# Performance work log

Measured on AMD Instinct MI355X. Metric: run time of the kernel, lower is better.

## Reference

```python
import jax, jax.numpy as jnp
import numpy as np

N_NODES = 100000
N_EDGES = 500000
N_GRAPHS = 64
IN_DIM = 512
HID = 256
N_REL = 16


def setup_inputs() -> dict:
    key = jax.random.key(0)
    ks = jax.random.split(key, 14)
    s = 0.02
    inp = {}
    inp["node_feats"] = jax.random.normal(ks[0], (N_NODES, IN_DIM), dtype=jnp.float32)
    inp["edge_index"] = jax.random.randint(ks[1], (2, N_EDGES), 0, N_NODES, dtype=jnp.int64)
    inp["batch_idx"] = jnp.sort(jax.random.randint(ks[2], (N_NODES,), 0, N_GRAPHS, dtype=jnp.int64))
    # GraphConv layer 0: in 512 -> 256; layers 1,2: 256 -> 256
    inp["W_rel0"] = jax.random.normal(ks[3], (IN_DIM, HID), dtype=jnp.float32) * s
    inp["W_root0"] = jax.random.normal(ks[4], (IN_DIM, HID), dtype=jnp.float32) * s
    inp["b0"] = jnp.zeros((HID,), dtype=jnp.float32)
    inp["W_rel1"] = jax.random.normal(ks[5], (HID, HID), dtype=jnp.float32) * s
    inp["W_root1"] = jax.random.normal(ks[6], (HID, HID), dtype=jnp.float32) * s
    inp["b1"] = jnp.zeros((HID,), dtype=jnp.float32)
    inp["W_rel2"] = jax.random.normal(ks[7], (HID, HID), dtype=jnp.float32) * s
    inp["W_root2"] = jax.random.normal(ks[8], (HID, HID), dtype=jnp.float32) * s
    inp["b2"] = jnp.zeros((HID,), dtype=jnp.float32)
    # edge head: concat(src, dst) -> relations
    inp["W_edge"] = jax.random.normal(ks[9], (2 * HID, N_REL), dtype=jnp.float32) * s
    inp["b_edge"] = jnp.zeros((N_REL,), dtype=jnp.float32)
    return inp


def _graph_conv(x, src, dst, W_rel, W_root, b):
    # PyG GraphConv: out_i = W_root x_i + W_rel * sum_{j in N(i)} x_j + b
    agg = jax.ops.segment_sum(x[src], dst, num_segments=x.shape[0])  # [N, d_in]
    return agg @ W_rel + x @ W_root + b


def reference(node_feats, edge_index, batch_idx,
              W_rel0, W_root0, b0, W_rel1, W_root1, b1, W_rel2, W_root2, b2,
              W_edge, b_edge):
    src, dst = edge_index[0], edge_index[1]
    # 3 GraphConv layers with ReLU (dropout is identity at inference)
    x = jax.nn.relu(_graph_conv(node_feats, src, dst, W_rel0, W_root0, b0))
    x = jax.nn.relu(_graph_conv(x, src, dst, W_rel1, W_root1, b1))
    x = jax.nn.relu(_graph_conv(x, src, dst, W_rel2, W_root2, b2))
    # edge head: gather src/dst embeddings, concat, linear
    edge_feats = jnp.concatenate([x[src], x[dst]], axis=1)  # [E, 2*HID]
    edge_logits = edge_feats @ W_edge + b_edge              # [E, N_REL]
    # global mean pool per graph
    sums = jax.ops.segment_sum(x, batch_idx, num_segments=N_GRAPHS)  # [G, HID]
    counts = jax.ops.segment_sum(jnp.ones((x.shape[0], 1), x.dtype), batch_idx, num_segments=N_GRAPHS)
    graph_embed = sums / jnp.maximum(counts, 1.0)
    return edge_logits, graph_embed
```

## Files before the change

kernel.cpp:

```cpp
#include <hip/hip_runtime.h>

#define N_NODES 100000
#define N_EDGES 500000
#define N_GRAPHS 64
#define IN_DIM 512
#define HID 256
#define NREL 16

using short8 = __attribute__((ext_vector_type(8))) short;
using f32x4  = __attribute__((ext_vector_type(4))) float;

__device__ __forceinline__ unsigned short f2bf(float f) {
    union { float f; unsigned u; } v; v.f = f;
    unsigned u = v.u;
    unsigned r = u + 0x7FFF + ((u >> 16) & 1);
    return (unsigned short)(r >> 16);
}
__device__ __forceinline__ float bf2f(unsigned short h) {
    union { unsigned u; float f; } v; v.u = ((unsigned)h) << 16;
    return v.f;
}

__device__ __forceinline__ void gload_lds16(const unsigned short* g, unsigned short* l) {
    __builtin_amdgcn_global_load_lds(
        (const __attribute__((address_space(1))) void*)(g),
        (__attribute__((address_space(3))) void*)(l), 16, 0, 0);
}

__global__ void k_f2bf(const float* __restrict__ in, unsigned short* __restrict__ out, int n8) {
    int i = blockIdx.x * 256 + threadIdx.x;
    if (i >= n8) return;
    const float4* p = (const float4*)in + (size_t)i * 2;
    float4 a = p[0], b = p[1];
    ushort4 u0, u1;
    u0.x = f2bf(a.x); u0.y = f2bf(a.y); u0.z = f2bf(a.z); u0.w = f2bf(a.w);
    u1.x = f2bf(b.x); u1.y = f2bf(b.y); u1.z = f2bf(b.z); u1.w = f2bf(b.w);
    ushort4* q = (ushort4*)out + (size_t)i * 2;
    q[0] = u0; q[1] = u1;
}

__global__ void k_makeWt(const float* __restrict__ Wrel, const float* __restrict__ Wroot,
                         unsigned short* __restrict__ Wt, int K) {
    int n = blockIdx.x;
    const float* Wsrc = (n < HID) ? Wrel : Wroot;
    int col = n & (HID - 1);
    for (int k = threadIdx.x; k < K; k += 256)
        Wt[(size_t)n * K + k] = f2bf(Wsrc[(size_t)k * HID + col]);
}

__global__ void k_makeWe2T(const float* __restrict__ We, unsigned short* __restrict__ We2T) {
    int idx = blockIdx.x * 256 + threadIdx.x;
    if (idx >= 32 * 256) return;
    int r = idx >> 8, k = idx & 255;
    float v = (r < 16) ? We[k * NREL + r] : We[(256 + k) * NREL + (r - 16)];
    We2T[idx] = f2bf(v);
}

__global__ void k_hist(const int* __restrict__ dstArr, int* __restrict__ counts) {
    int i = blockIdx.x * 256 + threadIdx.x;
    if (i < N_EDGES) atomicAdd(&counts[dstArr[i]], 1);
}

__global__ void k_scanA(const int* __restrict__ counts, int* __restrict__ bsum) {
    __shared__ int ws[4];
    int i = blockIdx.x * 256 + threadIdx.x;
    int v = (i < N_NODES) ? counts[i] : 0;
    for (int o = 32; o; o >>= 1) v += __shfl_down(v, o, 64);
    if ((threadIdx.x & 63) == 0) ws[threadIdx.x >> 6] = v;
    __syncthreads();
    if (threadIdx.x == 0) bsum[blockIdx.x] = ws[0] + ws[1] + ws[2] + ws[3];
}

__global__ void k_scanB(int* __restrict__ bsum, int nb) {
    __shared__ int buf[512];
    int t = threadIdx.x;
    for (int i = t; i < nb; i += 256) buf[i] = bsum[i];
    __syncthreads();
    if (t == 0) { int s = 0; for (int i = 0; i < nb; ++i) { int x = buf[i]; buf[i] = s; s += x; } }
    __syncthreads();
    for (int i = t; i < nb; i += 256) bsum[i] = buf[i];
}

__global__ void k_scanC(const int* __restrict__ counts, const int* __restrict__ bsum,
                        int* __restrict__ offsets, int* __restrict__ cur) {
    __shared__ int ws[4];
    int i = blockIdx.x * 256 + threadIdx.x;
    int lane = threadIdx.x & 63, wid = threadIdx.x >> 6;
    int v = (i < N_NODES) ? counts[i] : 0;
    int x = v;
    for (int o = 1; o < 64; o <<= 1) { int u = __shfl_up(x, o, 64); if (lane >= o) x += u; }
    if (lane == 63) ws[wid] = x;
    __syncthreads();
    if (threadIdx.x == 0) { int s = 0; for (int t = 0; t < 4; ++t) { int tt = ws[t]; ws[t] = s; s += tt; } }
    __syncthreads();
    x += ws[wid];
    x += bsum[blockIdx.x];
    if (i < N_NODES) { offsets[i + 1] = x; cur[i] = x - v; }
    if (i == 0) offsets[0] = 0;
}

__global__ void k_fill(const int* __restrict__ srcArr, const int* __restrict__ dstArr,
                       int* __restrict__ cur, int* __restrict__ csr) {
    int i = blockIdx.x * 256 + threadIdx.x;
    if (i < N_EDGES) {
        int p = atomicAdd(&cur[dstArr[i]], 1);
        csr[p] = srcArr[i];
    }
}

__global__ __launch_bounds__(256) void k_gemm(const unsigned short* __restrict__ A,
                                              const unsigned short* __restrict__ Bt,
                                              unsigned short* __restrict__ Yrel,
                                              unsigned short* __restrict__ Yroot,
                                              int M, int K) {
    __shared__ unsigned short lds[2 * 128 * 64];
    const int tid  = threadIdx.x;
    const int lane = tid & 63;
    const int w    = tid >> 6;
    const int wm   = w >> 1, wn = w & 1;

    int nwg  = gridDim.x;
    int orig = blockIdx.x;
    int q    = nwg >> 3;
    int id   = (orig & 7) * q + (orig >> 3);
    int bm0  = (id >> 2) * 128;
    int bn0  = (id & 3) * 128;

    f32x4 acc[4][4] = {};

    const int nkt = K >> 6;
    for (int kt = 0; kt < nkt; ++kt) {
        int k0 = kt << 6;
        #pragma unroll
        for (int it = 0; it < 4; ++it) {
            int c = (it << 8) + tid;
            int row = c >> 3, kcp = c & 7;
            int kcl = kcp ^ (row & 7);
            int gr = bm0 + row; gr = (gr < M) ? gr : (M - 1);
            gload_lds16(A + (size_t)gr * K + k0 + kcl * 8,
                        &lds[(size_t)((it << 8) + (w << 6)) * 8]);
        }
        #pragma unroll
        for (int it = 0; it < 4; ++it) {
            int c = (it << 8) + tid;
            int row = c >> 3, kcp = c & 7;
            int kcl = kcp ^ (row & 7);
            gload_lds16(Bt + (size_t)(bn0 + row) * K + k0 + kcl * 8,
                        &lds[128 * 64 + (size_t)((it << 8) + (w << 6)) * 8]);
        }
        __syncthreads();
        #pragma unroll
        for (int kk = 0; kk < 2; ++kk) {
            short8 af[4], bfr[4];
            #pragma unroll
            for (int m = 0; m < 4; ++m) {
                int row = wm * 64 + m * 16 + (lane & 15);
                int kcp = ((kk << 2) + (lane >> 4)) ^ (row & 7);
                af[m] = *(const short8*)&lds[row * 64 + kcp * 8];
            }
            #pragma unroll
            for (int n = 0; n < 4; ++n) {
                int row = wn * 64 + n * 16 + (lane & 15);
                int kcp = ((kk << 2) + (lane >> 4)) ^ (row & 7);
                bfr[n] = *(const short8*)&lds[128 * 64 + row * 64 + kcp * 8];
            }
            #pragma unroll
            for (int m = 0; m < 4; ++m)
                #pragma unroll
                for (int n = 0; n < 4; ++n)
                    acc[m][n] = __builtin_amdgcn_mfma_f32_16x16x32_bf16(af[m], bfr[n], acc[m][n], 0, 0, 0);
        }
        __syncthreads();
    }
    unsigned short* Cout = (bn0 < 256) ? Yrel : Yroot;
    int cb = bn0 & 255;
    #pragma unroll
    for (int m = 0; m < 4; ++m) {
        int row0 = bm0 + wm * 64 + m * 16 + ((lane >> 4) << 2);
        #pragma unroll
        for (int n = 0; n < 4; ++n) {
            int col = cb + wn * 64 + n * 16 + (lane & 15);
            #pragma unroll
            for (int i = 0; i < 4; ++i) {
                int r = row0 + i;
                if (r < M) Cout[(size_t)r * 256 + col] = f2bf(acc[m][n][i]);
            }
        }
    }
}

__global__ void k_combine(const unsigned short* __restrict__ yrel,
                          const unsigned short* __restrict__ yroot,
                          const int* __restrict__ offs,
                          const int* __restrict__ csr, const float* __restrict__ bias,
                          unsigned short* __restrict__ xout) {
    int node = blockIdx.x * 4 + (threadIdx.x >> 6);
    if (node >= N_NODES) return;
    int lane = threadIdx.x & 63;
    int d = lane * 4;
    float ax = 0.f, ay = 0.f, az = 0.f, aw = 0.f;
    int j0 = offs[node], j1 = offs[node + 1];
    for (int j = j0; j < j1; ++j) {
        int s = csr[j];
        ushort4 v = *(const ushort4*)(yrel + (size_t)s * 256 + d);
        ax += bf2f(v.x); ay += bf2f(v.y); az += bf2f(v.z); aw += bf2f(v.w);
    }
    ushort4 rr = *(const ushort4*)(yroot + (size_t)node * 256 + d);
    float4 bb = *(const float4*)(bias + d);
    ushort4 pk;
    pk.x = f2bf(fmaxf(ax + bf2f(rr.x) + bb.x, 0.f));
    pk.y = f2bf(fmaxf(ay + bf2f(rr.y) + bb.y, 0.f));
    pk.z = f2bf(fmaxf(az + bf2f(rr.z) + bb.z, 0.f));
    pk.w = f2bf(fmaxf(aw + bf2f(rr.w) + bb.w, 0.f));
    *(ushort4*)(xout + (size_t)node * HID + d) = pk;
}

__global__ void k_proj(const unsigned short* __restrict__ x,
                       const unsigned short* __restrict__ We2T,
                       float* __restrict__ P) {
    int lane = threadIdx.x & 63;
    int g = blockIdx.x * 4 + (threadIdx.x >> 6);
    if (g * 16 >= N_NODES) return;
    int n0 = g * 16;
    short8 bfr[2][8];
    #pragma unroll
    for (int cg = 0; cg < 2; ++cg)
        #pragma unroll
        for (int ks = 0; ks < 8; ++ks)
            bfr[cg][ks] = *(const short8*)&We2T[(size_t)(cg * 16 + (lane & 15)) * 256 + ks * 32 + ((lane >> 4) << 3)];
    f32x4 acc[2] = {};
    const size_t rb = (size_t)(n0 + (lane & 15)) * 256 + ((lane >> 4) << 3);
    #pragma unroll
    for (int ks = 0; ks < 8; ++ks) {
        short8 af = *(const short8*)&x[rb + ks * 32];
        acc[0] = __builtin_amdgcn_mfma_f32_16x16x32_bf16(af, bfr[0][ks], acc[0], 0, 0, 0);
        acc[1] = __builtin_amdgcn_mfma_f32_16x16x32_bf16(af, bfr[1][ks], acc[1], 0, 0, 0);
    }
    #pragma unroll
    for (int cg = 0; cg < 2; ++cg) {
        #pragma unroll
        for (int i = 0; i < 4; ++i) {
            int n = n0 + ((lane >> 4) << 2) + i;
            P[(size_t)n * 32 + cg * 16 + (lane & 15)] = acc[cg][i];
        }
    }
}

__global__ void k_edge_add(const float* __restrict__ P,
                           const int* __restrict__ srcArr, const int* __restrict__ dstArr,
                           const float* __restrict__ b_edge, float* __restrict__ out) {
    int e = blockIdx.x * 256 + threadIdx.x;
    if (e >= N_EDGES) return;
    int s = srcArr[e], d = dstArr[e];
    const float4* ps = (const float4*)(P + (size_t)s * 32);
    const float4* pd = (const float4*)(P + (size_t)d * 32 + 16);
    const float4* bb = (const float4*)b_edge;
    float4* po = (float4*)(out + (size_t)e * 16);
    #pragma unroll
    for (int i = 0; i < 4; ++i) {
        float4 a = ps[i], b = pd[i], c = bb[i];
        float4 r;
        r.x = a.x + b.x + c.x; r.y = a.y + b.y + c.y;
        r.z = a.z + b.z + c.z; r.w = a.w + b.w + c.w;
        po[i] = r;
    }
}

__global__ void k_pool_sum(const unsigned short* __restrict__ x, const int* __restrict__ batch,
                           float* __restrict__ sums) {
    const int CH = 32;
    int w = threadIdx.x >> 6, lane = threadIdx.x & 63;
    int n0 = blockIdx.x * (4 * CH) + w * CH;
    if (n0 >= N_NODES) return;
    int n1 = n0 + CH; if (n1 > N_NODES) n1 = N_NODES;
    int d = lane * 4;
    float a0 = 0.f, a1 = 0.f, a2 = 0.f, a3 = 0.f;
    int gcur = batch[n0];
    for (int n = n0; n < n1; ++n) {
        int g = batch[n];
        if (g != gcur) {
            float* p = &sums[gcur * HID + d];
            atomicAdd(p + 0, a0); atomicAdd(p + 1, a1);
            atomicAdd(p + 2, a2); atomicAdd(p + 3, a3);
            a0 = a1 = a2 = a3 = 0.f; gcur = g;
        }
        ushort4 v = *(const ushort4*)&x[(size_t)n * HID + d];
        a0 += bf2f(v.x); a1 += bf2f(v.y); a2 += bf2f(v.z); a3 += bf2f(v.w);
    }
    float* p = &sums[gcur * HID + d];
    atomicAdd(p + 0, a0); atomicAdd(p + 1, a1);
    atomicAdd(p + 2, a2); atomicAdd(p + 3, a3);
}

__device__ __forceinline__ int lowerBound(const int* a, int n, int key) {
    int lo = 0, hi = n;
    while (lo < hi) { int mid = (lo + hi) >> 1; if (a[mid] < key) lo = mid + 1; else hi = mid; }
    return lo;
}

__global__ void k_pool_final(const float* __restrict__ sums, const int* __restrict__ batch,
                             float* __restrict__ out) {
    int g = blockIdx.x, d = threadIdx.x;
    int lo = lowerBound(batch, N_NODES, g);
    int hi = lowerBound(batch, N_NODES, g + 1);
    float cnt = (float)(hi - lo);
    out[(size_t)g * HID + d] = sums[g * HID + d] / fmaxf(cnt, 1.0f);
}

extern "C" void kernel_launch(void* const* d_in, const int* in_sizes, int n_in,
                              void* d_out, int out_size, void* d_ws, size_t ws_size,
                              hipStream_t stream) {
    const float* node_feats = (const float*)d_in[0];
    const int*   edge_index = (const int*)d_in[1];
    const int*   batch_idx  = (const int*)d_in[2];
    const float* W_rel0  = (const float*)d_in[3];
    const float* W_root0 = (const float*)d_in[4];
    const float* b0      = (const float*)d_in[5];
    const float* W_rel1  = (const float*)d_in[6];
    const float* W_root1 = (const float*)d_in[7];
    const float* b1      = (const float*)d_in[8];
    const float* W_rel2  = (const float*)d_in[9];
    const float* W_root2 = (const float*)d_in[10];
    const float* b2      = (const float*)d_in[11];
    const float* W_edge  = (const float*)d_in[12];
    const float* b_edge  = (const float*)d_in[13];

    const int* src = edge_index;
    const int* dst = edge_index + N_EDGES;

    char* ws = (char*)d_ws;
    size_t off = 0;
    auto alloc = [&](size_t bytes) -> char* {
        off = (off + 255) & ~(size_t)255;
        char* p = ws + off;
        off += bytes;
        return p;
    };
    unsigned short* bufA  = (unsigned short*)alloc((size_t)N_NODES * IN_DIM * 2);
    unsigned short* bufB  = (unsigned short*)alloc((size_t)N_NODES * HID * 2);
    unsigned short* Yrel  = (unsigned short*)alloc((size_t)N_NODES * HID * 2);
    unsigned short* Yroot = (unsigned short*)alloc((size_t)N_NODES * HID * 2);
    unsigned short* Wt0   = (unsigned short*)alloc(512 * 512 * 2);
    unsigned short* Wt1   = (unsigned short*)alloc(512 * 256 * 2);
    unsigned short* Wt2   = (unsigned short*)alloc(512 * 256 * 2);
    unsigned short* We2T  = (unsigned short*)alloc(32 * 256 * 2);
    float* P     = (float*)alloc((size_t)N_NODES * 32 * 4);
    int* counts  = (int*)alloc((size_t)N_NODES * 4);
    int* offsets = (int*)alloc((size_t)(N_NODES + 1) * 4);
    int* cur     = (int*)alloc((size_t)N_NODES * 4);
    int* csr     = (int*)alloc((size_t)N_EDGES * 4);
    int* bsum    = (int*)alloc(512 * 4);
    float* sums  = (float*)alloc(N_GRAPHS * HID * 4);

    const int nscan = (N_NODES + 255) / 256;

    hipMemsetAsync(counts, 0, (size_t)N_NODES * 4, stream);
    hipMemsetAsync(sums, 0, N_GRAPHS * HID * 4, stream);

    k_f2bf<<<(N_NODES * IN_DIM / 8 + 255) / 256, 256, 0, stream>>>(node_feats, bufA, N_NODES * IN_DIM / 8);
    k_makeWt<<<512, 256, 0, stream>>>(W_rel0, W_root0, Wt0, 512);
    k_makeWt<<<512, 256, 0, stream>>>(W_rel1, W_root1, Wt1, 256);
    k_makeWt<<<512, 256, 0, stream>>>(W_rel2, W_root2, Wt2, 256);
    k_makeWe2T<<<32, 256, 0, stream>>>(W_edge, We2T);

    k_hist<<<(N_EDGES + 255) / 256, 256, 0, stream>>>(dst, counts);
    k_scanA<<<nscan, 256, 0, stream>>>(counts, bsum);
    k_scanB<<<1, 256, 0, stream>>>(bsum, nscan);
    k_scanC<<<nscan, 256, 0, stream>>>(counts, bsum, offsets, cur);
    k_fill<<<(N_EDGES + 255) / 256, 256, 0, stream>>>(src, dst, cur, csr);

    const int gemmGrid = ((N_NODES + 127) / 128) * 4;
    k_gemm<<<gemmGrid, 256, 0, stream>>>(bufA, Wt0, Yrel, Yroot, N_NODES, 512);
    k_combine<<<(N_NODES + 3) / 4, 256, 0, stream>>>(Yrel, Yroot, offsets, csr, b0, bufB);
    k_gemm<<<gemmGrid, 256, 0, stream>>>(bufB, Wt1, Yrel, Yroot, N_NODES, 256);
    k_combine<<<(N_NODES + 3) / 4, 256, 0, stream>>>(Yrel, Yroot, offsets, csr, b1, bufA);
    k_gemm<<<gemmGrid, 256, 0, stream>>>(bufA, Wt2, Yrel, Yroot, N_NODES, 256);
    k_combine<<<(N_NODES + 3) / 4, 256, 0, stream>>>(Yrel, Yroot, offsets, csr, b2, bufB);

    float* out_logits = (float*)d_out;
    k_proj<<<(N_NODES / 16 + 3) / 4, 256, 0, stream>>>(bufB, We2T, P);
    k_edge_add<<<(N_EDGES + 255) / 256, 256, 0, stream>>>(P, src, dst, b_edge, out_logits);

    float* out_embed = (float*)d_out + (size_t)N_EDGES * NREL;
    k_pool_sum<<<(N_NODES + 127) / 128, 256, 0, stream>>>(bufB, batch_idx, sums);
    k_pool_final<<<N_GRAPHS, 256, 0, stream>>>(sums, batch_idx, out_embed);
}
```

Before: 591.5 us.

## Rewrite node GEMM with 256x128 tiles, 512 threads and triple-buffered LDS pipeline

Replaces the single-buffered 128x128 GEMM with a templated kernel that uses 256-row tiles, 8 waves per block, and a 3-slot LDS ring. Global-to-LDS loads are issued two k-steps ahead, with explicit vmcnt waits and raw barriers. MFMA issue priority is raised during the compute section. The XCD block remapping now handles grids not divisible by 8. The aim is to hide global load latency and improve B-tile reuse, at the cost of more LDS per block (144KB), which limits occupancy.

```diff
diff --git a/kernel.cpp b/kernel.cpp
--- a/kernel.cpp
+++ b/kernel.cpp
@@ -108,70 +108,93 @@
     }
 }
 
-__global__ __launch_bounds__(256) void k_gemm(const unsigned short* __restrict__ A,
-                                              const unsigned short* __restrict__ Bt,
-                                              unsigned short* __restrict__ Yrel,
-                                              unsigned short* __restrict__ Yroot,
-                                              int M, int K) {
-    __shared__ unsigned short lds[2 * 128 * 64];
+template<int KDIM>
+__global__ __launch_bounds__(512, 2) void k_gemm2(const unsigned short* __restrict__ A,
+                                                  const unsigned short* __restrict__ Bt,
+                                                  unsigned short* __restrict__ Yrel,
+                                                  unsigned short* __restrict__ Yroot,
+                                                  int M) {
+    __shared__ unsigned short lds[3 * 24576];
+    constexpr int NKT = KDIM / 64;
     const int tid  = threadIdx.x;
     const int lane = tid & 63;
     const int w    = tid >> 6;
-    const int wm   = w >> 1, wn = w & 1;
-
-    int nwg  = gridDim.x;
-    int orig = blockIdx.x;
-    int q    = nwg >> 3;
-    int id   = (orig & 7) * q + (orig >> 3);
-    int bm0  = (id >> 2) * 128;
-    int bn0  = (id & 3) * 128;
-
-    f32x4 acc[4][4] = {};
-
-    const int nkt = K >> 6;
-    for (int kt = 0; kt < nkt; ++kt) {
-        int k0 = kt << 6;
+    const int wm   = w >> 1;
+    const int wn   = w & 1;
+
+    int nwg = gridDim.x, orig = blockIdx.x;
+    int q = nwg >> 3, r = nwg & 7;
+    int xcd = orig & 7, local = orig >> 3;
+    int id = (xcd < r ? xcd * (q + 1) : r * (q + 1) + (xcd - r) * q) + local;
+    int bm0 = (id >> 2) * 256;
+    int bn0 = (id & 3) * 128;
+
+    auto stage = [&](int slot, int kt) {
+        unsigned short* sA = lds + slot * 24576;
+        unsigned short* sB = sA + 16384;
+        const int k0 = kt << 6;
         #pragma unroll
         for (int it = 0; it < 4; ++it) {
-            int c = (it << 8) + tid;
+            int c = (it << 9) + tid;
             int row = c >> 3, kcp = c & 7;
             int kcl = kcp ^ (row & 7);
-            int gr = bm0 + row; gr = (gr < M) ? gr : (M - 1);
-            gload_lds16(A + (size_t)gr * K + k0 + kcl * 8,
-                        &lds[(size_t)((it << 8) + (w << 6)) * 8]);
-        }
-        #pragma unroll
-        for (int it = 0; it < 4; ++it) {
-            int c = (it << 8) + tid;
+            int gr = bm0 + row; if (gr >= M) gr = M - 1;
+            gload_lds16(A + (size_t)gr * KDIM + k0 + kcl * 8,
+                        sA + (size_t)((it << 9) + (w << 6)) * 8);
+        }
+        #pragma unroll
+        for (int it = 0; it < 2; ++it) {
+            int c = (it << 9) + tid;
             int row = c >> 3, kcp = c & 7;
             int kcl = kcp ^ (row & 7);
-            gload_lds16(Bt + (size_t)(bn0 + row) * K + k0 + kcl * 8,
-                        &lds[128 * 64 + (size_t)((it << 8) + (w << 6)) * 8]);
-        }
-        __syncthreads();
+            gload_lds16(Bt + (size_t)(bn0 + row) * KDIM + k0 + kcl * 8,
+                        sB + (size_t)((it << 9) + (w << 6)) * 8);
+        }
+    };
+
+    f32x4 acc[4][4] = {};
+
+    stage(0, 0);
+    stage(1, 1);
+
+    #pragma unroll
+    for (int kt = 0; kt < NKT; ++kt) {
+        if (kt + 2 < NKT) stage((kt + 2) % 3, kt + 2);
+        if (kt + 2 < NKT)      asm volatile("s_waitcnt vmcnt(12)" ::: "memory");
+        else if (kt + 1 < NKT) asm volatile("s_waitcnt vmcnt(6)"  ::: "memory");
+        else                   asm volatile("s_waitcnt vmcnt(0)"  ::: "memory");
+        __builtin_amdgcn_s_barrier();
+        __builtin_amdgcn_sched_barrier(0);
+
+        const unsigned short* sA = lds + (kt % 3) * 24576;
+        const unsigned short* sB = sA + 16384;
         #pragma unroll
         for (int kk = 0; kk < 2; ++kk) {
             short8 af[4], bfr[4];
             #pragma unroll
             for (int m = 0; m < 4; ++m) {
                 int row = wm * 64 + m * 16 + (lane & 15);
-                int kcp = ((kk << 2) + (lane >> 4)) ^ (row & 7);
-                af[m] = *(const short8*)&lds[row * 64 + kcp * 8];
+                int g = ((kk << 2) + (lane >> 4)) ^ (row & 7);
+                af[m] = *(const short8*)&sA[row * 64 + g * 8];
             }
             #pragma unroll
             for (int n = 0; n < 4; ++n) {
                 int row = wn * 64 + n * 16 + (lane & 15);
-                int kcp = ((kk << 2) + (lane >> 4)) ^ (row & 7);
-                bfr[n] = *(const short8*)&lds[128 * 64 + row * 64 + kcp * 8];
+                int g = ((kk << 2) + (lane >> 4)) ^ (row & 7);
+                bfr[n] = *(const short8*)&sB[row * 64 + g * 8];
             }
+            __builtin_amdgcn_s_setprio(1);
             #pragma unroll
             for (int m = 0; m < 4; ++m)
                 #pragma unroll
                 for (int n = 0; n < 4; ++n)
                     acc[m][n] = __builtin_amdgcn_mfma_f32_16x16x32_bf16(af[m], bfr[n], acc[m][n], 0, 0, 0);
-        }
-        __syncthreads();
-    }
+            __builtin_amdgcn_s_setprio(0);
+        }
+        __builtin_amdgcn_s_barrier();
+        __builtin_amdgcn_sched_barrier(0);
+    }
+
     unsigned short* Cout = (bn0 < 256) ? Yrel : Yroot;
     int cb = bn0 & 255;
     #pragma unroll
@@ -182,8 +205,8 @@
             int col = cb + wn * 64 + n * 16 + (lane & 15);
             #pragma unroll
             for (int i = 0; i < 4; ++i) {
-                int r = row0 + i;
-                if (r < M) Cout[(size_t)r * 256 + col] = f2bf(acc[m][n][i]);
+                int rr = row0 + i;
+                if (rr < M) Cout[(size_t)rr * 256 + col] = f2bf(acc[m][n][i]);
             }
         }
     }
@@ -259,10 +282,10 @@
     #pragma unroll
     for (int i = 0; i < 4; ++i) {
         float4 a = ps[i], b = pd[i], c = bb[i];
-        float4 r;
-        r.x = a.x + b.x + c.x; r.y = a.y + b.y + c.y;
-        r.z = a.z + b.z + c.z; r.w = a.w + b.w + c.w;
-        po[i] = r;
+        float4 rr;
+        rr.x = a.x + b.x + c.x; rr.y = a.y + b.y + c.y;
+        rr.z = a.z + b.z + c.z; rr.w = a.w + b.w + c.w;
+        po[i] = rr;
     }
 }
 
@@ -369,12 +392,12 @@
     k_scanC<<<nscan, 256, 0, stream>>>(counts, bsum, offsets, cur);
     k_fill<<<(N_EDGES + 255) / 256, 256, 0, stream>>>(src, dst, cur, csr);
 
-    const int gemmGrid = ((N_NODES + 127) / 128) * 4;
-    k_gemm<<<gemmGrid, 256, 0, stream>>>(bufA, Wt0, Yrel, Yroot, N_NODES, 512);
+    const int gemmGrid = ((N_NODES + 255) / 256) * 4;
+    k_gemm2<512><<<gemmGrid, 512, 0, stream>>>(bufA, Wt0, Yrel, Yroot, N_NODES);
     k_combine<<<(N_NODES + 3) / 4, 256, 0, stream>>>(Yrel, Yroot, offsets, csr, b0, bufB);
-    k_gemm<<<gemmGrid, 256, 0, stream>>>(bufB, Wt1, Yrel, Yroot, N_NODES, 256);
+    k_gemm2<256><<<gemmGrid, 512, 0, stream>>>(bufB, Wt1, Yrel, Yroot, N_NODES);
     k_combine<<<(N_NODES + 3) / 4, 256, 0, stream>>>(Yrel, Yroot, offsets, csr, b1, bufA);
-    k_gemm<<<gemmGrid, 256, 0, stream>>>(bufA, Wt2, Yrel, Yroot, N_NODES, 256);
+    k_gemm2<256><<<gemmGrid, 512, 0, stream>>>(bufA, Wt2, Yrel, Yroot, N_NODES);
     k_combine<<<(N_NODES + 3) / 4, 256, 0, stream>>>(Yrel, Yroot, offsets, csr, b2, bufB);
 
     float* out_logits = (float*)d_out;
```

Measured after the change: 605.8 us. 1.02x slower.

## Fuse fp32-to-bf16 input conversion into first GEMM, tile weight transpose, unroll gather

Applied to the files above, without the earlier changes.

Adds a first-layer GEMM that reads fp32 node features directly, converts them to bf16 in registers and writes them swizzled into LDS. This removes the separate conversion kernel and its 100MB bf16 intermediate round trip. The weight-transpose kernel now uses a shared-memory tiled transpose for coalesced reads, and the combine gather loop is unrolled by four with independent accumulators to expose memory-level parallelism. In exchange, the A-tile loads in the first GEMM become synchronous register loads with conversion instead of async direct-to-LDS loads, which may reduce load/compute overlap in that kernel.

```diff
diff --git a/kernel.cpp b/kernel.cpp
--- a/kernel.cpp
+++ b/kernel.cpp
@@ -27,25 +27,26 @@
         (__attribute__((address_space(3))) void*)(l), 16, 0, 0);
 }
 
-__global__ void k_f2bf(const float* __restrict__ in, unsigned short* __restrict__ out, int n8) {
-    int i = blockIdx.x * 256 + threadIdx.x;
-    if (i >= n8) return;
-    const float4* p = (const float4*)in + (size_t)i * 2;
-    float4 a = p[0], b = p[1];
-    ushort4 u0, u1;
-    u0.x = f2bf(a.x); u0.y = f2bf(a.y); u0.z = f2bf(a.z); u0.w = f2bf(a.w);
-    u1.x = f2bf(b.x); u1.y = f2bf(b.y); u1.z = f2bf(b.z); u1.w = f2bf(b.w);
-    ushort4* q = (ushort4*)out + (size_t)i * 2;
-    q[0] = u0; q[1] = u1;
-}
-
 __global__ void k_makeWt(const float* __restrict__ Wrel, const float* __restrict__ Wroot,
                          unsigned short* __restrict__ Wt, int K) {
-    int n = blockIdx.x;
-    const float* Wsrc = (n < HID) ? Wrel : Wroot;
-    int col = n & (HID - 1);
-    for (int k = threadIdx.x; k < K; k += 256)
-        Wt[(size_t)n * K + k] = f2bf(Wsrc[(size_t)k * HID + col]);
+    __shared__ float t[64][65];
+    int tid = threadIdx.x;
+    int tk = blockIdx.x * 64, tn = blockIdx.y * 64;
+    const float* Wsrc = (tn < 256) ? Wrel : Wroot;
+    int col0 = tn & 255;
+    #pragma unroll
+    for (int r = 0; r < 16; ++r) {
+        int kl = r * 4 + (tid >> 6);
+        int nl = tid & 63;
+        t[kl][nl] = Wsrc[(size_t)(tk + kl) * 256 + col0 + nl];
+    }
+    __syncthreads();
+    #pragma unroll
+    for (int r = 0; r < 16; ++r) {
+        int nl = r * 4 + (tid >> 6);
+        int kl = tid & 63;
+        Wt[(size_t)(tn + nl) * K + tk + kl] = f2bf(t[kl][nl]);
+    }
 }
 
 __global__ void k_makeWe2T(const float* __restrict__ We, unsigned short* __restrict__ We2T) {
@@ -155,14 +156,14 @@
             #pragma unroll
             for (int m = 0; m < 4; ++m) {
                 int row = wm * 64 + m * 16 + (lane & 15);
-                int kcp = ((kk << 2) + (lane >> 4)) ^ (row & 7);
-                af[m] = *(const short8*)&lds[row * 64 + kcp * 8];
+                int g = ((kk << 2) + (lane >> 4)) ^ (row & 7);
+                af[m] = *(const short8*)&lds[row * 64 + g * 8];
             }
             #pragma unroll
             for (int n = 0; n < 4; ++n) {
                 int row = wn * 64 + n * 16 + (lane & 15);
-                int kcp = ((kk << 2) + (lane >> 4)) ^ (row & 7);
-                bfr[n] = *(const short8*)&lds[128 * 64 + row * 64 + kcp * 8];
+                int g = ((kk << 2) + (lane >> 4)) ^ (row & 7);
+                bfr[n] = *(const short8*)&lds[128 * 64 + row * 64 + g * 8];
             }
             #pragma unroll
             for (int m = 0; m < 4; ++m)
@@ -187,6 +188,95 @@
             }
         }
     }
+}
+
+__global__ __launch_bounds__(256) void k_gemm0(const float* __restrict__ A,
+                                               const unsigned short* __restrict__ Bt,
+                                               unsigned short* __restrict__ Yrel,
+                                               unsigned short* __restrict__ Yroot,
+                                               int M) {
+    constexpr int K = 512;
+    __shared__ unsigned short lds[2 * 128 * 64];
+    const int tid  = threadIdx.x;
+    const int lane = tid & 63;
+    const int w    = tid >> 6;
+    const int wm   = w >> 1, wn = w & 1;
+
+    int nwg  = gridDim.x;
+    int orig = blockIdx.x;
+    int q    = nwg >> 3;
+    int id   = (orig & 7) * q + (orig >> 3);
+    int bm0  = (id >> 2) * 128;
+    int bn0  = (id & 3) * 128;
+
+    f32x4 acc[4][4] = {};
+
+    const int nkt = K >> 6;
+    for (int kt = 0; kt < nkt; ++kt) {
+        int k0 = kt << 6;
+        #pragma unroll
+        for (int it = 0; it < 4; ++it) {
+            int c = (it << 8) + tid;
+            int row = c >> 3, kcp = c & 7;
+            int kcl = kcp ^ (row & 7);
+            gload_lds16(Bt + (size_t)(bn0 + row) * K + k0 + kcl * 8,
+                        &lds[128 * 64 + (size_t)((it << 8) + (w << 6)) * 8]);
+        }
+        #pragma unroll
+        for (int it = 0; it < 8; ++it) {
+            int c = (it << 8) + tid;
+            int row = c >> 4;
+            int f4  = c & 15;
+            int gr = bm0 + row; gr = (gr < M) ? gr : (M - 1);
+            float4 v = *(const float4*)(A + (size_t)gr * K + k0 + f4 * 4);
+            ushort4 u;
+            u.x = f2bf(v.x); u.y = f2bf(v.y); u.z = f2bf(v.z); u.w = f2bf(v.w);
+            int g = (f4 >> 1) ^ (row & 7);
+            *(ushort4*)&lds[row * 64 + g * 8 + (f4 & 1) * 4] = u;
+        }
+        __syncthreads();
+        #pragma unroll
+        for (int kk = 0; kk < 2; ++kk) {
+            short8 af[4], bfr[4];
+            #pragma unroll
+            for (int m = 0; m < 4; ++m) {
+                int row = wm * 64 + m * 16 + (lane & 15);
+                int g = ((kk << 2) + (lane >> 4)) ^ (row & 7);
+                af[m] = *(const short8*)&lds[row * 64 + g * 8];
+            }
+            #pragma unroll
+            for (int n = 0; n < 4; ++n) {
+                int row = wn * 64 + n * 16 + (lane & 15);
+                int g = ((kk << 2) + (lane >> 4)) ^ (row & 7);
+                bfr[n] = *(const short8*)&lds[128 * 64 + row * 64 + g * 8];
+            }
+            #pragma unroll
+            for (int m = 0; m < 4; ++m)
+                #pragma unroll
+                for (int n = 0; n < 4; ++n)
+                    acc[m][n] = __builtin_amdgcn_mfma_f32_16x16x32_bf16(af[m], bfr[n], acc[m][n], 0, 0, 0);
+        }
+        __syncthreads();
+    }
+    unsigned short* Cout = (bn0 < 256) ? Yrel : Yroot;
+    int cb = bn0 & 255;
+    #pragma unroll
+    for (int m = 0; m < 4; ++m) {
+        int row0 = bm0 + wm * 64 + m * 16 + ((lane >> 4) << 2);
+        #pragma unroll
+        for (int n = 0; n < 4; ++n) {
+            int col = cb + wn * 64 + n * 16 + (lane & 15);
+            #pragma unroll
+            for (int i = 0; i < 4; ++i) {
+                int r = row0 + i;
+                if (r < M) Cout[(size_t)r * 256 + col] = f2bf(acc[m][n][i]);
+            }
+        }
+    }
+}
+
+__device__ __forceinline__ void acc4(float4& a, ushort4 v) {
+    a.x += bf2f(v.x); a.y += bf2f(v.y); a.z += bf2f(v.z); a.w += bf2f(v.w);
 }
 
 __global__ void k_combine(const unsigned short* __restrict__ yrel,
@@ -198,20 +288,32 @@
     if (node >= N_NODES) return;
     int lane = threadIdx.x & 63;
     int d = lane * 4;
-    float ax = 0.f, ay = 0.f, az = 0.f, aw = 0.f;
     int j0 = offs[node], j1 = offs[node + 1];
-    for (int j = j0; j < j1; ++j) {
+    float4 a0 = {0,0,0,0}, a1 = {0,0,0,0}, a2 = {0,0,0,0}, a3 = {0,0,0,0};
+    int j = j0;
+    for (; j + 4 <= j1; j += 4) {
+        int s0 = csr[j], s1 = csr[j + 1], s2 = csr[j + 2], s3 = csr[j + 3];
+        ushort4 v0 = *(const ushort4*)(yrel + (size_t)s0 * 256 + d);
+        ushort4 v1 = *(const ushort4*)(yrel + (size_t)s1 * 256 + d);
+        ushort4 v2 = *(const ushort4*)(yrel + (size_t)s2 * 256 + d);
+        ushort4 v3 = *(const ushort4*)(yrel + (size_t)s3 * 256 + d);
+        acc4(a0, v0); acc4(a1, v1); acc4(a2, v2); acc4(a3, v3);
+    }
+    for (; j < j1; ++j) {
         int s = csr[j];
-        ushort4 v = *(const ushort4*)(yrel + (size_t)s * 256 + d);
-        ax += bf2f(v.x); ay += bf2f(v.y); az += bf2f(v.z); aw += bf2f(v.w);
-    }
+        acc4(a0, *(const ushort4*)(yrel + (size_t)s * 256 + d));
+    }
+    a0.x += a1.x + a2.x + a3.x;
+    a0.y += a1.y + a2.y + a3.y;
+    a0.z += a1.z + a2.z + a3.z;
+    a0.w += a1.w + a2.w + a3.w;
     ushort4 rr = *(const ushort4*)(yroot + (size_t)node * 256 + d);
     float4 bb = *(const float4*)(bias + d);
     ushort4 pk;
-    pk.x = f2bf(fmaxf(ax + bf2f(rr.x) + bb.x, 0.f));
-    pk.y = f2bf(fmaxf(ay + bf2f(rr.y) + bb.y, 0.f));
-    pk.z = f2bf(fmaxf(az + bf2f(rr.z) + bb.z, 0.f));
-    pk.w = f2bf(fmaxf(aw + bf2f(rr.w) + bb.w, 0.f));
+    pk.x = f2bf(fmaxf(a0.x + bf2f(rr.x) + bb.x, 0.f));
+    pk.y = f2bf(fmaxf(a0.y + bf2f(rr.y) + bb.y, 0.f));
+    pk.z = f2bf(fmaxf(a0.z + bf2f(rr.z) + bb.z, 0.f));
+    pk.w = f2bf(fmaxf(a0.w + bf2f(rr.w) + bb.w, 0.f));
     *(ushort4*)(xout + (size_t)node * HID + d) = pk;
 }
 
@@ -259,10 +361,10 @@
     #pragma unroll
     for (int i = 0; i < 4; ++i) {
         float4 a = ps[i], b = pd[i], c = bb[i];
-        float4 r;
-        r.x = a.x + b.x + c.x; r.y = a.y + b.y + c.y;
-        r.z = a.z + b.z + c.z; r.w = a.w + b.w + c.w;
-        po[i] = r;
+        float4 rr;
+        rr.x = a.x + b.x + c.x; rr.y = a.y + b.y + c.y;
+        rr.z = a.z + b.z + c.z; rr.w = a.w + b.w + c.w;
+        po[i] = rr;
     }
 }
 
@@ -336,8 +438,8 @@
         off += bytes;
         return p;
     };
-    unsigned short* bufA  = (unsigned short*)alloc((size_t)N_NODES * IN_DIM * 2);
-    unsigned short* bufB  = (unsigned short*)alloc((size_t)N_NODES * HID * 2);
+    unsigned short* xA    = (unsigned short*)alloc((size_t)N_NODES * HID * 2);
+    unsigned short* xB    = (unsigned short*)alloc((size_t)N_NODES * HID * 2);
     unsigned short* Yrel  = (unsigned short*)alloc((size_t)N_NODES * HID * 2);
     unsigned short* Yroot = (unsigned short*)alloc((size_t)N_NODES * HID * 2);
     unsigned short* Wt0   = (unsigned short*)alloc(512 * 512 * 2);
@@ -357,10 +459,9 @@
     hipMemsetAsync(counts, 0, (size_t)N_NODES * 4, stream);
     hipMemsetAsync(sums, 0, N_GRAPHS * HID * 4, stream);
 
-    k_f2bf<<<(N_NODES * IN_DIM / 8 + 255) / 256, 256, 0, stream>>>(node_feats, bufA, N_NODES * IN_DIM / 8);
-    k_makeWt<<<512, 256, 0, stream>>>(W_rel0, W_root0, Wt0, 512);
-    k_makeWt<<<512, 256, 0, stream>>>(W_rel1, W_root1, Wt1, 256);
-    k_makeWt<<<512, 256, 0, stream>>>(W_rel2, W_root2, Wt2, 256);
+    k_makeWt<<<dim3(8, 8), 256, 0, stream>>>(W_rel0, W_root0, Wt0, 512);
+    k_makeWt<<<dim3(4, 8), 256, 0, stream>>>(W_rel1, W_root1, Wt1, 256);
+    k_makeWt<<<dim3(4, 8), 256, 0, stream>>>(W_rel2, W_root2, Wt2, 256);
     k_makeWe2T<<<32, 256, 0, stream>>>(W_edge, We2T);
 
     k_hist<<<(N_EDGES + 255) / 256, 256, 0, stream>>>(dst, counts);
@@ -370,18 +471,18 @@
     k_fill<<<(N_EDGES + 255) / 256, 256, 0, stream>>>(src, dst, cur, csr);
 
     const int gemmGrid = ((N_NODES + 127) / 128) * 4;
-    k_gemm<<<gemmGrid, 256, 0, stream>>>(bufA, Wt0, Yrel, Yroot, N_NODES, 512);
-    k_combine<<<(N_NODES + 3) / 4, 256, 0, stream>>>(Yrel, Yroot, offsets, csr, b0, bufB);
-    k_gemm<<<gemmGrid, 256, 0, stream>>>(bufB, Wt1, Yrel, Yroot, N_NODES, 256);
-    k_combine<<<(N_NODES + 3) / 4, 256, 0, stream>>>(Yrel, Yroot, offsets, csr, b1, bufA);
-    k_gemm<<<gemmGrid, 256, 0, stream>>>(bufA, Wt2, Yrel, Yroot, N_NODES, 256);
-    k_combine<<<(N_NODES + 3) / 4, 256, 0, stream>>>(Yrel, Yroot, offsets, csr, b2, bufB);
+    k_gemm0<<<gemmGrid, 256, 0, stream>>>(node_feats, Wt0, Yrel, Yroot, N_NODES);
+    k_combine<<<(N_NODES + 3) / 4, 256, 0, stream>>>(Yrel, Yroot, offsets, csr, b0, xB);
+    k_gemm<<<gemmGrid, 256, 0, stream>>>(xB, Wt1, Yrel, Yroot, N_NODES, 256);
+    k_combine<<<(N_NODES + 3) / 4, 256, 0, stream>>>(Yrel, Yroot, offsets, csr, b1, xA);
+    k_gemm<<<gemmGrid, 256, 0, stream>>>(xA, Wt2, Yrel, Yroot, N_NODES, 256);
+    k_combine<<<(N_NODES + 3) / 4, 256, 0, stream>>>(Yrel, Yroot, offsets, csr, b2, xB);
 
     float* out_logits = (float*)d_out;
-    k_proj<<<(N_NODES / 16 + 3) / 4, 256, 0, stream>>>(bufB, We2T, P);
+    k_proj<<<(N_NODES / 16 + 3) / 4, 256, 0, stream>>>(xB, We2T, P);
     k_edge_add<<<(N_EDGES + 255) / 256, 256, 0, stream>>>(P, src, dst, b_edge, out_logits);
 
     float* out_embed = (float*)d_out + (size_t)N_EDGES * NREL;
-    k_pool_sum<<<(N_NODES + 127) / 128, 256, 0, stream>>>(bufB, batch_idx, sums);
+    k_pool_sum<<<(N_NODES + 127) / 128, 256, 0, stream>>>(xB, batch_idx, sums);
     k_pool_final<<<N_GRAPHS, 256, 0, stream>>>(sums, batch_idx, out_embed);
 }
```

Result: faster. 544.8 us (-7.9%).
